# Optimization experiments

Measured on AMD Instinct MI355X. Metric: run time of the kernel, lower is better.

The kernel has to match this reference:

```python
import jax, jax.numpy as jnp
import numpy as np

N_NODES = 50000
NEG_SLOPE = 0.2

def _segment_softmax(e, seg, n):
    m = jax.ops.segment_max(e, seg, num_segments=n)
    ex = jnp.exp(e - m[seg])
    s = jax.ops.segment_sum(ex, seg, num_segments=n)
    return ex / s[seg]

def _gatv2_layer(x, src, dst, n, Wl, bl, Wr, br, att):
    # GATv2 (heads=1): e_ij = att . leaky_relu(Wl x_j + Wr x_i); msg = alpha * Wl x_j
    xl = x @ Wl + bl            # [N, D] source transform
    xr = x @ Wr + br            # [N, D] target transform
    h = jax.nn.leaky_relu(xl[src] + xr[dst], NEG_SLOPE)  # [E, D]
    e = h @ att                 # [E]
    alpha = _segment_softmax(e, dst, n)
    out = jax.ops.segment_sum(alpha[:, None] * xl[src], dst, num_segments=n)
    return out

def setup_inputs() -> dict:
    key = jax.random.key(0)
    ks = jax.random.split(key, 16)
    N, E, Q, F, D, H = N_NODES, 800000, 200000, 128, 250, 256
    def glorot(k, shape):
        fan = shape[0] + shape[-1]
        return jax.random.uniform(k, shape, jnp.float32, -1.0, 1.0) * np.sqrt(6.0 / fan)
    return {
        "x": jax.random.normal(ks[0], (N, F), jnp.float32),
        "edge_index": jax.random.randint(ks[1], (2, E), 0, N, jnp.int32),
        "query": jax.random.randint(ks[2], (Q, 2), 0, N, jnp.int32),
        "W1l": glorot(ks[3], (F, D)), "b1l": jnp.zeros((D,), jnp.float32),
        "W1r": glorot(ks[4], (F, D)), "b1r": jnp.zeros((D,), jnp.float32),
        "att1": glorot(ks[5], (D,)),
        "W2l": glorot(ks[6], (D, D)), "b2l": jnp.zeros((D,), jnp.float32),
        "W2r": glorot(ks[7], (D, D)), "b2r": jnp.zeros((D,), jnp.float32),
        "att2": glorot(ks[8], (D,)),
        "Wm1": glorot(ks[9], (2 * D, H)), "bm1": jnp.zeros((H,), jnp.float32),
        "Wm2": glorot(ks[10], (H, 1)), "bm2": jnp.zeros((1,), jnp.float32),
    }

def reference(x, edge_index, query, W1l, b1l, W1r, b1r, att1,
              W2l, b2l, W2r, b2r, att2, Wm1, bm1, Wm2, bm2):
    n = x.shape[0]
    # add self loops (PyG default add_self_loops=True)
    loops = jnp.arange(n, dtype=edge_index.dtype)
    src = jnp.concatenate([edge_index[0], loops])
    dst = jnp.concatenate([edge_index[1], loops])
    h = _gatv2_layer(x, src, dst, n, W1l, b1l, W1r, b1r, att1)
    h = jax.nn.relu(h)
    emb = _gatv2_layer(h, src, dst, n, W2l, b2l, W2r, b2r, att2)
    # edge-prediction head: gather pair embeddings, concat, MLP
    pair = jnp.concatenate([emb[query[:, 0]], emb[query[:, 1]]], axis=1)  # [Q, 2D]
    out = jax.nn.relu(pair @ Wm1 + bm1)
    out = jax.nn.relu(out @ Wm2 + bm2)
    return out
```

## Files before the change

### kernel.cpp

```cpp
#include <hip/hip_runtime.h>
#include <hip/hip_fp16.h>
#include <math.h>
#include <stdint.h>

#define NN 50000
#define NE 800000
#define ET (NE + NN)
#define FIN 128
#define DD 250
#define HD 256
#define NQ 200000
#define NEG_SLOPE 0.2f

typedef unsigned short u16;
typedef __attribute__((ext_vector_type(4))) float f32x4;
typedef _Float16 h2v __attribute__((ext_vector_type(2)));
typedef _Float16 f16x8 __attribute__((ext_vector_type(8)));

union H2U { h2v h; unsigned int u; };

__device__ __forceinline__ u16 f2h(float v) {
    __half h = __float2half(v);
    return *reinterpret_cast<u16*>(&h);
}
__device__ __forceinline__ float4 ld4h(const u16* p) {
    uint2 r = *(const uint2*)p;
    __half2 a = *(__half2*)&r.x;
    __half2 b = *(__half2*)&r.y;
    float2 fa = __half22float2(a), fb = __half22float2(b);
    return make_float4(fa.x, fa.y, fb.x, fb.y);
}
__device__ __forceinline__ h2v hmax2v(h2v a, h2v b) {
    return __builtin_elementwise_max(a, b);
}


__global__ void count_kernel(const int* __restrict__ ei, int* __restrict__ cnt) {
    int k = blockIdx.x * 256 + threadIdx.x;
    if (k >= ET) return;
    int d = (k < NE) ? ei[NE + k] : (k - NE);
    atomicAdd(&cnt[d], 1);
}

__global__ __launch_bounds__(256) void scan1_kernel(
    int* __restrict__ cnt, int* __restrict__ rowptr, int* __restrict__ bsum)
{
    __shared__ int buf[256];
    int t = threadIdx.x;
    int i = blockIdx.x * 256 + t;
    int v = (i < NN) ? cnt[i] : 0;
    if (i < NN) cnt[i] = 0;
    buf[t] = v;
    __syncthreads();
#pragma unroll
    for (int off = 1; off < 256; off <<= 1) {
        int add = (t >= off) ? buf[t - off] : 0;
        __syncthreads();
        buf[t] += add;
        __syncthreads();
    }
    if (i < NN) rowptr[i] = buf[t] - v;
    if (t == 255) bsum[blockIdx.x] = buf[255];
}

__global__ __launch_bounds__(256) void scan2_kernel(
    int* __restrict__ bsum, int* __restrict__ rowptr, int nb)
{
    __shared__ int buf[256];
    int t = threadIdx.x;
    int v = (t < nb) ? bsum[t] : 0;
    buf[t] = v;
    __syncthreads();
#pragma unroll
    for (int off = 1; off < 256; off <<= 1) {
        int add = (t >= off) ? buf[t - off] : 0;
        __syncthreads();
        buf[t] += add;
        __syncthreads();
    }
    if (t < nb) bsum[t] = buf[t] - v;
    if (t == 255) rowptr[NN] = buf[255];
}

__global__ __launch_bounds__(256) void scan3_kernel(
    int* __restrict__ rowptr, const int* __restrict__ bsum)
{
    int i = blockIdx.x * 256 + threadIdx.x;
    if (i < NN) rowptr[i] += bsum[blockIdx.x];
}

__global__ void scatter_kernel(const int* __restrict__ ei,
                               const int* __restrict__ rowptr,
                               int* __restrict__ fill,
                               int* __restrict__ ssrc) {
    int k = blockIdx.x * 256 + threadIdx.x;
    if (k >= ET) return;
    int s, d;
    if (k < NE) { s = ei[k]; d = ei[NE + k]; }
    else        { s = k - NE; d = k - NE; }
    int pos = rowptr[d] + atomicAdd(&fill[d], 1);
    ssrc[pos] = s << 9;
}


#define CONVX_BLOCKS 3125

__global__ __launch_bounds__(256) void conv_all(
    const float* __restrict__ x, int* __restrict__ fill,
    u16* __restrict__ Asp,
    const float* __restrict__ W1l, const float* __restrict__ W1r,
    const float* __restrict__ W2l, const float* __restrict__ W2r,
    const float* __restrict__ Wm1,
    u16* __restrict__ W1lT, u16* __restrict__ W1rT,
    u16* __restrict__ W2lT, u16* __restrict__ W2rT,
    u16* __restrict__ WmtT, u16* __restrict__ WmbT)
{
    if (blockIdx.x < CONVX_BLOCKS) {
        int tid = blockIdx.x * 256 + threadIdx.x;
        if (tid < NN) fill[tid] = 0;
        size_t idx = (size_t)tid * 8;
        if (idx >= (size_t)NN * FIN) return;
        float4 v0 = *(const float4*)(x + idx);
        float4 v1 = *(const float4*)(x + idx + 4);
        ushort4 o0, o1;
        o0.x = f2h(v0.x); o0.y = f2h(v0.y); o0.z = f2h(v0.z); o0.w = f2h(v0.w);
        o1.x = f2h(v1.x); o1.y = f2h(v1.y); o1.z = f2h(v1.z); o1.w = f2h(v1.w);
        *(ushort4*)(Asp + idx) = o0;
        *(ushort4*)(Asp + idx + 4) = o1;
        return;
    }
    int b = blockIdx.x - CONVX_BLOCKS;
    const float* W; int K, N, koff, kshift, b0; u16* ot;
    if (b < 128)       { W = W1l; K = FIN; N = DD; koff = 0;  kshift = 7; b0 = 0;    ot = W1lT; }
    else if (b < 256)  { W = W1r; K = FIN; N = DD; koff = 0;  kshift = 7; b0 = 128;  ot = W1rT; }
    else if (b < 512)  { W = W2l; K = DD;  N = DD; koff = 0;  kshift = 8; b0 = 256;  ot = W2lT; }
    else if (b < 768)  { W = W2r; K = DD;  N = DD; koff = 0;  kshift = 8; b0 = 512;  ot = W2rT; }
    else if (b < 1024) { W = Wm1; K = DD;  N = HD; koff = 0;  kshift = 8; b0 = 768;  ot = WmtT; }
    else               { W = Wm1; K = DD;  N = HD; koff = DD; kshift = 8; b0 = 1024; ot = WmbT; }
    int id = (b - b0) * 256 + threadIdx.x;
    int Kp = 1 << kshift;
    int n = id >> kshift, k = id & (Kp - 1);
    float v = (n < N && k < K) ? W[(size_t)(k + koff) * N + n] : 0.f;
    ot[id] = f2h(v);
}


#define AP 40

__global__ __launch_bounds__(256, 2) void gemm_pair(
    const u16* __restrict__ A, int Kp,
    const u16* __restrict__ B0, const u16* __restrict__ B1,
    const float* __restrict__ bias0, const float* __restrict__ bias1,
    void* __restrict__ C0v, void* __restrict__ C1v, int M, int N, int fmt)
{
    __shared__ u16 AS[128][AP], B0S[128][AP], B1S[128][AP];

    int row0 = blockIdx.x * 128;
    int col0 = blockIdx.y * 128;
    int t = threadIdx.x;
    int lane = t & 63, w = t >> 6;
    int wr = w >> 1, wc = w & 1;
    int quad = lane >> 4, rr = lane & 15;

    f32x4 acc0[4][4], acc1[4][4];
#pragma unroll
    for (int i = 0; i < 4; i++)
#pragma unroll
        for (int j = 0; j < 4; j++) {
            acc0[i][j] = (f32x4){0.f, 0.f, 0.f, 0.f};
            acc1[i][j] = (f32x4){0.f, 0.f, 0.f, 0.f};
        }

    int ar = t >> 1, akh = (t & 1) * 16;
    int gr = row0 + ar;
    int nB = col0 + ar;
    const u16* pA  = A  + (size_t)gr * Kp + akh;
    const u16* pB0 = B0 + (size_t)nB * Kp + akh;
    const u16* pB1 = B1 + (size_t)nB * Kp + akh;

    for (int k0 = 0; k0 < Kp; k0 += 32) {
        f16x8 a0{}, a1{};
        if (gr < M) {
            a0 = *(const f16x8*)(pA + k0);
            a1 = *(const f16x8*)(pA + k0 + 8);
        }
        *(f16x8*)&AS[ar][akh]      = a0;
        *(f16x8*)&AS[ar][akh + 8]  = a1;
        *(f16x8*)&B0S[ar][akh]     = *(const f16x8*)(pB0 + k0);
        *(f16x8*)&B0S[ar][akh + 8] = *(const f16x8*)(pB0 + k0 + 8);
        *(f16x8*)&B1S[ar][akh]     = *(const f16x8*)(pB1 + k0);
        *(f16x8*)&B1S[ar][akh + 8] = *(const f16x8*)(pB1 + k0 + 8);
        __syncthreads();

        f16x8 fA[4];
#pragma unroll
        for (int fi = 0; fi < 4; fi++) {
            int r = wr * 64 + fi * 16 + rr;
            fA[fi] = *(const f16x8*)&AS[r][quad * 8];
        }
#pragma unroll
        for (int fj = 0; fj < 4; fj++) {
            int c = wc * 64 + fj * 16 + rr;
            f16x8 b0 = *(const f16x8*)&B0S[c][quad * 8];
            f16x8 b1 = *(const f16x8*)&B1S[c][quad * 8];
#pragma unroll
            for (int fi = 0; fi < 4; fi++) {
                acc0[fi][fj] = __builtin_amdgcn_mfma_f32_16x16x32_f16(fA[fi], b0, acc0[fi][fj], 0, 0, 0);
                acc1[fi][fj] = __builtin_amdgcn_mfma_f32_16x16x32_f16(fA[fi], b1, acc1[fi][fj], 0, 0, 0);
            }
        }
        __syncthreads();
    }

#pragma unroll
    for (int fj = 0; fj < 4; fj++) {
        int gc = col0 + wc * 64 + fj * 16 + rr;
        if (gc >= N) continue;
        float bb0 = bias0 ? bias0[gc] : 0.f;
        float bb1 = bias1 ? bias1[gc] : 0.f;
#pragma unroll
        for (int fi = 0; fi < 4; fi++) {
#pragma unroll
            for (int r = 0; r < 4; r++) {
                int grr = row0 + wr * 64 + fi * 16 + quad * 4 + r;
                if (grr < M) {
                    float v0 = acc0[fi][fj][r] + bb0;
                    float v1 = acc1[fi][fj][r] + bb1;
                    if (fmt & 1) ((u16*)C0v)[(size_t)grr * 256 + gc] = f2h(v0);
                    else         ((float*)C0v)[(size_t)grr * N + gc] = v0;
                    if (fmt & 2) ((u16*)C1v)[(size_t)grr * 256 + gc] = f2h(v1);
                    else         ((float*)C1v)[(size_t)grr * N + gc] = v1;
                }
            }
        }
    }
}


__global__ __launch_bounds__(256) void fused_edge_kernel(
    const int* __restrict__ rowptr, const int* __restrict__ ssrc,
    const u16* __restrict__ xl16, const u16* __restrict__ xr16,
    const float* __restrict__ att,
    u16* __restrict__ Oh, int dorelu)
{
    int i = blockIdx.x * 4 + (threadIdx.x >> 6);
    if (i >= NN) return;
    int lane = threadIdx.x & 63;
    int beg = __builtin_amdgcn_readfirstlane(rowptr[i]);
    int end = __builtin_amdgcn_readfirstlane(rowptr[i + 1]);
    int d0 = lane * 4;
    int lb = d0 * 2;

    uint2 xrr = *(const uint2*)&xr16[(size_t)i * 256 + d0];
    h2v xr0h = *(h2v*)&xrr.x, xr1h = *(h2v*)&xrr.y;
    float atf[4] = {0.f, 0.f, 0.f, 0.f};
#pragma unroll
    for (int j = 0; j < 4; j++)
        if (d0 + j < DD) atf[j] = att[d0 + j];
    h2v at0h, at1h;
    at0h.x = (_Float16)atf[0]; at0h.y = (_Float16)atf[1];
    at1h.x = (_Float16)atf[2]; at1h.y = (_Float16)atf[3];
    const h2v c02 = {(_Float16)0.2f, (_Float16)0.2f};

    const char* xlb = (const char*)xl16;

    float m = -1e30f, ssum = 0.f;
    float4 acc = make_float4(0.f, 0.f, 0.f, 0.f);

    int p = beg;
    for (; p + 3 < end; p += 4) {
        int o0 = __builtin_amdgcn_readfirstlane(ssrc[p]);
        int o1 = __builtin_amdgcn_readfirstlane(ssrc[p + 1]);
        int o2 = __builtin_amdgcn_readfirstlane(ssrc[p + 2]);
        int o3 = __builtin_amdgcn_readfirstlane(ssrc[p + 3]);
        uint2 r0 = *(const uint2*)(xlb + o0 + lb);
        uint2 r1 = *(const uint2*)(xlb + o1 + lb);
        uint2 r2 = *(const uint2*)(xlb + o2 + lb);
        uint2 r3 = *(const uint2*)(xlb + o3 + lb);
        h2v x00 = *(h2v*)&r0.x, x01 = *(h2v*)&r0.y;
        h2v x10 = *(h2v*)&r1.x, x11 = *(h2v*)&r1.y;
        h2v x20 = *(h2v*)&r2.x, x21 = *(h2v*)&r2.y;
        h2v x30 = *(h2v*)&r3.x, x31 = *(h2v*)&r3.y;

        h2v s;
        float e0, e1, e2, e3;
        s = x00 + xr0h; s = hmax2v(s, s * c02);
        e0 = __builtin_amdgcn_fdot2(s, at0h, 0.f, false);
        s = x01 + xr1h; s = hmax2v(s, s * c02);
        e0 = __builtin_amdgcn_fdot2(s, at1h, e0, false);
        s = x10 + xr0h; s = hmax2v(s, s * c02);
        e1 = __builtin_amdgcn_fdot2(s, at0h, 0.f, false);
        s = x11 + xr1h; s = hmax2v(s, s * c02);
        e1 = __builtin_amdgcn_fdot2(s, at1h, e1, false);
        s = x20 + xr0h; s = hmax2v(s, s * c02);
        e2 = __builtin_amdgcn_fdot2(s, at0h, 0.f, false);
        s = x21 + xr1h; s = hmax2v(s, s * c02);
        e2 = __builtin_amdgcn_fdot2(s, at1h, e2, false);
        s = x30 + xr0h; s = hmax2v(s, s * c02);
        e3 = __builtin_amdgcn_fdot2(s, at0h, 0.f, false);
        s = x31 + xr1h; s = hmax2v(s, s * c02);
        e3 = __builtin_amdgcn_fdot2(s, at1h, e3, false);

        H2U u01, u23;
        u01.h.x = (_Float16)e0; u01.h.y = (_Float16)e1;
        u23.h.x = (_Float16)e2; u23.h.y = (_Float16)e3;
#pragma unroll
        for (int off = 1; off < 64; off <<= 1) {
            H2U t01, t23;
            t01.u = (unsigned int)__shfl_xor((int)u01.u, off, 64);
            t23.u = (unsigned int)__shfl_xor((int)u23.u, off, 64);
            u01.h = u01.h + t01.h;
            u23.h = u23.h + t23.h;
        }
        float es0 = (float)u01.h.x, es1 = (float)u01.h.y;
        float es2 = (float)u23.h.x, es3 = (float)u23.h.y;

        float nm = fmaxf(fmaxf(m, es0), fmaxf(fmaxf(es1, es2), es3));
        float sc = __expf(m - nm);
        float w0 = __expf(es0 - nm);
        float w1 = __expf(es1 - nm);
        float w2 = __expf(es2 - nm);
        float w3 = __expf(es3 - nm);
        float ax0 = fmaf(w1, (float)x10.x, w0 * (float)x00.x);
        float ax1 = fmaf(w3, (float)x30.x, w2 * (float)x20.x);
        float ay0 = fmaf(w1, (float)x10.y, w0 * (float)x00.y);
        float ay1 = fmaf(w3, (float)x30.y, w2 * (float)x20.y);
        float az0 = fmaf(w1, (float)x11.x, w0 * (float)x01.x);
        float az1 = fmaf(w3, (float)x31.x, w2 * (float)x21.x);
        float aw0 = fmaf(w1, (float)x11.y, w0 * (float)x01.y);
        float aw1 = fmaf(w3, (float)x31.y, w2 * (float)x21.y);
        acc.x = fmaf(acc.x, sc, ax0 + ax1);
        acc.y = fmaf(acc.y, sc, ay0 + ay1);
        acc.z = fmaf(acc.z, sc, az0 + az1);
        acc.w = fmaf(acc.w, sc, aw0 + aw1);
        ssum = fmaf(ssum, sc, (w0 + w1) + (w2 + w3));
        m = nm;
    }
    for (; p < end; p++) {
        int o = __builtin_amdgcn_readfirstlane(ssrc[p]);
        uint2 r = *(const uint2*)(xlb + o + lb);
        h2v x0 = *(h2v*)&r.x, x1 = *(h2v*)&r.y;
        h2v s;
        float e;
        s = x0 + xr0h; s = hmax2v(s, s * c02);
        e = __builtin_amdgcn_fdot2(s, at0h, 0.f, false);
        s = x1 + xr1h; s = hmax2v(s, s * c02);
        e = __builtin_amdgcn_fdot2(s, at1h, e, false);
#pragma unroll
        for (int off = 1; off < 64; off <<= 1)
            e += __shfl_xor(e, off, 64);
        float nm = fmaxf(m, e);
        float sc = __expf(m - nm);
        float w = __expf(e - nm);
        acc.x = fmaf(w, (float)x0.x, acc.x * sc);
        acc.y = fmaf(w, (float)x0.y, acc.y * sc);
        acc.z = fmaf(w, (float)x1.x, acc.z * sc);
        acc.w = fmaf(w, (float)x1.y, acc.w * sc);
        ssum = fmaf(ssum, sc, w);
        m = nm;
    }

    float inv = 1.f / ssum;
    acc.x *= inv; acc.y *= inv; acc.z *= inv; acc.w *= inv;
    if (dorelu) {
        acc.x = fmaxf(acc.x, 0.f); acc.y = fmaxf(acc.y, 0.f);
        acc.z = fmaxf(acc.z, 0.f); acc.w = fmaxf(acc.w, 0.f);
    }
    size_t base = (size_t)i * 256 + d0;
    ushort4 hv;
    hv.x = f2h(acc.x); hv.y = f2h(acc.y); hv.z = f2h(acc.z); hv.w = f2h(acc.w);
    *(ushort4*)&Oh[base] = hv;
}


__global__ __launch_bounds__(256) void query_kernel(
    const int* __restrict__ qry, const u16* __restrict__ Ptop,
    const u16* __restrict__ Pbot, const float* __restrict__ Wm2,
    const float* __restrict__ bm2, float* __restrict__ out)
{
    int q = (blockIdx.x * 4 + (threadIdx.x >> 6)) * 2;
    if (q >= NQ) return;
    int lane = threadIdx.x & 63;
    int a0 = __builtin_amdgcn_readfirstlane(qry[q * 2 + 0]);
    int b0 = __builtin_amdgcn_readfirstlane(qry[q * 2 + 1]);
    int a1 = __builtin_amdgcn_readfirstlane(qry[q * 2 + 2]);
    int b1 = __builtin_amdgcn_readfirstlane(qry[q * 2 + 3]);
    float4 w  = *(const float4*)&Wm2[lane * 4];
    float4 t0 = ld4h(&Ptop[(size_t)a0 * HD + lane * 4]);
    float4 v0 = ld4h(&Pbot[(size_t)b0 * HD + lane * 4]);
    float4 t1 = ld4h(&Ptop[(size_t)a1 * HD + lane * 4]);
    float4 v1 = ld4h(&Pbot[(size_t)b1 * HD + lane * 4]);
    float s0 = fmaxf(t0.x + v0.x, 0.f) * w.x + fmaxf(t0.y + v0.y, 0.f) * w.y
             + fmaxf(t0.z + v0.z, 0.f) * w.z + fmaxf(t0.w + v0.w, 0.f) * w.w;
    float s1 = fmaxf(t1.x + v1.x, 0.f) * w.x + fmaxf(t1.y + v1.y, 0.f) * w.y
             + fmaxf(t1.z + v1.z, 0.f) * w.z + fmaxf(t1.w + v1.w, 0.f) * w.w;
#pragma unroll
    for (int off = 32; off > 0; off >>= 1) {
        s0 += __shfl_down(s0, off, 64);
        s1 += __shfl_down(s1, off, 64);
    }
    if (lane == 0) {
        float bb = bm2[0];
        out[q] = fmaxf(s0 + bb, 0.f);
        if (q + 1 < NQ) out[q + 1] = fmaxf(s1 + bb, 0.f);
    }
}


extern "C" void kernel_launch(void* const* d_in, const int* in_sizes, int n_in,
                              void* d_out, int out_size, void* d_ws, size_t ws_size,
                              hipStream_t stream) {
    const float* x    = (const float*)d_in[0];
    const int*   ei   = (const int*)d_in[1];
    const int*   qry  = (const int*)d_in[2];
    const float* W1l  = (const float*)d_in[3];
    const float* b1l  = (const float*)d_in[4];
    const float* W1r  = (const float*)d_in[5];
    const float* b1r  = (const float*)d_in[6];
    const float* att1 = (const float*)d_in[7];
    const float* W2l  = (const float*)d_in[8];
    const float* b2l  = (const float*)d_in[9];
    const float* W2r  = (const float*)d_in[10];
    const float* b2r  = (const float*)d_in[11];
    const float* att2 = (const float*)d_in[12];
    const float* Wm1  = (const float*)d_in[13];
    const float* bm1  = (const float*)d_in[14];
    const float* Wm2  = (const float*)d_in[15];
    const float* bm2  = (const float*)d_in[16];
    float* out = (float*)d_out;

    u16* xl16    = (u16*)d_ws;
    u16* xr16    = xl16 + (size_t)NN * 256;
    int* rowptr  = (int*)(xr16 + (size_t)NN * 256);
    int* fill    = rowptr + NN + 1;
    int* ssrc    = fill + NN;
    int* bsum    = ssrc + ET;
    uintptr_t wp = (uintptr_t)(bsum + 256);
    wp = (wp + 63) & ~(uintptr_t)63;
    u16* W1lT = (u16*)wp;
    u16* W1rT = W1lT + 256 * 128;
    u16* W2lT = W1rT + 256 * 128;
    u16* W2rT = W2lT + 65536;
    u16* WmtT = W2rT + 65536;
    u16* WmbT = WmtT + 65536;
    u16* Asp  = WmbT + 65536;
    u16* Ptop16 = xl16;
    u16* Pbot16 = xr16;

    dim3 blk(256);
    int gET = (ET + 255) / 256;
    int gNode = (NN + 3) / 4;
    int nb = (NN + 255) / 256;
    dim3 gg((NN + 127) / 128, 2);

    conv_all<<<CONVX_BLOCKS + 1280, blk, 0, stream>>>(x, fill, Asp,
        W1l, W1r, W2l, W2r, Wm1,
        W1lT, W1rT, W2lT, W2rT, WmtT, WmbT);

    count_kernel<<<gET, blk, 0, stream>>>(ei, fill);
    scan1_kernel<<<nb, blk, 0, stream>>>(fill, rowptr, bsum);
    scan2_kernel<<<1, blk, 0, stream>>>(bsum, rowptr, nb);
    scan3_kernel<<<nb, blk, 0, stream>>>(rowptr, bsum);
    scatter_kernel<<<gET, blk, 0, stream>>>(ei, rowptr, fill, ssrc);

    gemm_pair<<<gg, blk, 0, stream>>>(Asp, 128, W1lT, W1rT,
                                      b1l, b1r, (void*)xl16, (void*)xr16, NN, DD, 3);
    fused_edge_kernel<<<gNode, blk, 0, stream>>>(rowptr, ssrc, xl16, xr16, att1, Asp, 1);

    gemm_pair<<<gg, blk, 0, stream>>>(Asp, 256, W2lT, W2rT,
                                      b2l, b2r, (void*)xl16, (void*)xr16, NN, DD, 3);
    fused_edge_kernel<<<gNode, blk, 0, stream>>>(rowptr, ssrc, xl16, xr16, att2, Asp, 0);

    gemm_pair<<<gg, blk, 0, stream>>>(Asp, 256, WmtT, WmbT,
                                      bm1, (const float*)nullptr, (void*)Ptop16, (void*)Pbot16, NN, HD, 3);

    query_kernel<<<(NQ / 2 + 3) / 4, blk, 0, stream>>>(qry, Ptop16, Pbot16, Wm2, bm2, out);
}
```

Before: 523.3 us.

## Software-pipeline edge gathers and use DPP wave reductions in aggregation

The per-node aggregation loop now prefetches the next group of four source rows and the following group's indices while computing the current group, so gather latency overlaps with the score and softmax math. The xor-shuffle butterfly reductions are replaced by DPP row shifts and row broadcasts followed by a readlane of lane 63, which avoids LDS-based shuffles. The query head uses the same DPP reduction. The 1-3 leftover edges are processed with their loads issued together. This raises register pressure and adds more complex control flow.

```diff
diff --git a/kernel.cpp b/kernel.cpp
--- a/kernel.cpp
+++ b/kernel.cpp
@@ -32,6 +32,34 @@
 }
 __device__ __forceinline__ h2v hmax2v(h2v a, h2v b) {
     return __builtin_elementwise_max(a, b);
+}
+
+
+#define DPPMOV(v, ctrl, rm) \
+    ((unsigned int)__builtin_amdgcn_update_dpp(0, (int)(v), (ctrl), (rm), 0xF, true))
+
+__device__ __forceinline__ unsigned int h2_wave_sum63(h2v x) {
+    H2U u, t; u.h = x;
+    t.u = DPPMOV(u.u, 0x111, 0xF); u.h = u.h + t.h;
+    t.u = DPPMOV(u.u, 0x112, 0xF); u.h = u.h + t.h;
+    t.u = DPPMOV(u.u, 0x114, 0xF); u.h = u.h + t.h;
+    t.u = DPPMOV(u.u, 0x118, 0xF); u.h = u.h + t.h;
+    t.u = DPPMOV(u.u, 0x142, 0xA); u.h = u.h + t.h;
+    t.u = DPPMOV(u.u, 0x143, 0xC); u.h = u.h + t.h;
+    return (unsigned int)__builtin_amdgcn_readlane((int)u.u, 63);
+}
+
+__device__ __forceinline__ float f32_wave_sum63(float x) {
+    union FU { float f; unsigned int u; } a, t, o;
+    a.f = x;
+    t.u = DPPMOV(a.u, 0x111, 0xF); a.f += t.f;
+    t.u = DPPMOV(a.u, 0x112, 0xF); a.f += t.f;
+    t.u = DPPMOV(a.u, 0x114, 0xF); a.f += t.f;
+    t.u = DPPMOV(a.u, 0x118, 0xF); a.f += t.f;
+    t.u = DPPMOV(a.u, 0x142, 0xA); a.f += t.f;
+    t.u = DPPMOV(a.u, 0x143, 0xC); a.f += t.f;
+    o.u = (unsigned int)__builtin_amdgcn_readlane((int)a.u, 63);
+    return o.f;
 }
 
 
@@ -267,88 +295,19 @@
     float m = -1e30f, ssum = 0.f;
     float4 acc = make_float4(0.f, 0.f, 0.f, 0.f);
 
-    int p = beg;
-    for (; p + 3 < end; p += 4) {
-        int o0 = __builtin_amdgcn_readfirstlane(ssrc[p]);
-        int o1 = __builtin_amdgcn_readfirstlane(ssrc[p + 1]);
-        int o2 = __builtin_amdgcn_readfirstlane(ssrc[p + 2]);
-        int o3 = __builtin_amdgcn_readfirstlane(ssrc[p + 3]);
-        uint2 r0 = *(const uint2*)(xlb + o0 + lb);
-        uint2 r1 = *(const uint2*)(xlb + o1 + lb);
-        uint2 r2 = *(const uint2*)(xlb + o2 + lb);
-        uint2 r3 = *(const uint2*)(xlb + o3 + lb);
-        h2v x00 = *(h2v*)&r0.x, x01 = *(h2v*)&r0.y;
-        h2v x10 = *(h2v*)&r1.x, x11 = *(h2v*)&r1.y;
-        h2v x20 = *(h2v*)&r2.x, x21 = *(h2v*)&r2.y;
-        h2v x30 = *(h2v*)&r3.x, x31 = *(h2v*)&r3.y;
-
-        h2v s;
-        float e0, e1, e2, e3;
-        s = x00 + xr0h; s = hmax2v(s, s * c02);
-        e0 = __builtin_amdgcn_fdot2(s, at0h, 0.f, false);
-        s = x01 + xr1h; s = hmax2v(s, s * c02);
-        e0 = __builtin_amdgcn_fdot2(s, at1h, e0, false);
-        s = x10 + xr0h; s = hmax2v(s, s * c02);
-        e1 = __builtin_amdgcn_fdot2(s, at0h, 0.f, false);
-        s = x11 + xr1h; s = hmax2v(s, s * c02);
-        e1 = __builtin_amdgcn_fdot2(s, at1h, e1, false);
-        s = x20 + xr0h; s = hmax2v(s, s * c02);
-        e2 = __builtin_amdgcn_fdot2(s, at0h, 0.f, false);
-        s = x21 + xr1h; s = hmax2v(s, s * c02);
-        e2 = __builtin_amdgcn_fdot2(s, at1h, e2, false);
-        s = x30 + xr0h; s = hmax2v(s, s * c02);
-        e3 = __builtin_amdgcn_fdot2(s, at0h, 0.f, false);
-        s = x31 + xr1h; s = hmax2v(s, s * c02);
-        e3 = __builtin_amdgcn_fdot2(s, at1h, e3, false);
-
-        H2U u01, u23;
-        u01.h.x = (_Float16)e0; u01.h.y = (_Float16)e1;
-        u23.h.x = (_Float16)e2; u23.h.y = (_Float16)e3;
-#pragma unroll
-        for (int off = 1; off < 64; off <<= 1) {
-            H2U t01, t23;
-            t01.u = (unsigned int)__shfl_xor((int)u01.u, off, 64);
-            t23.u = (unsigned int)__shfl_xor((int)u23.u, off, 64);
-            u01.h = u01.h + t01.h;
-            u23.h = u23.h + t23.h;
-        }
-        float es0 = (float)u01.h.x, es1 = (float)u01.h.y;
-        float es2 = (float)u23.h.x, es3 = (float)u23.h.y;
-
-        float nm = fmaxf(fmaxf(m, es0), fmaxf(fmaxf(es1, es2), es3));
-        float sc = __expf(m - nm);
-        float w0 = __expf(es0 - nm);
-        float w1 = __expf(es1 - nm);
-        float w2 = __expf(es2 - nm);
-        float w3 = __expf(es3 - nm);
-        float ax0 = fmaf(w1, (float)x10.x, w0 * (float)x00.x);
-        float ax1 = fmaf(w3, (float)x30.x, w2 * (float)x20.x);
-        float ay0 = fmaf(w1, (float)x10.y, w0 * (float)x00.y);
-        float ay1 = fmaf(w3, (float)x30.y, w2 * (float)x20.y);
-        float az0 = fmaf(w1, (float)x11.x, w0 * (float)x01.x);
-        float az1 = fmaf(w3, (float)x31.x, w2 * (float)x21.x);
-        float aw0 = fmaf(w1, (float)x11.y, w0 * (float)x01.y);
-        float aw1 = fmaf(w3, (float)x31.y, w2 * (float)x21.y);
-        acc.x = fmaf(acc.x, sc, ax0 + ax1);
-        acc.y = fmaf(acc.y, sc, ay0 + ay1);
-        acc.z = fmaf(acc.z, sc, az0 + az1);
-        acc.w = fmaf(acc.w, sc, aw0 + aw1);
-        ssum = fmaf(ssum, sc, (w0 + w1) + (w2 + w3));
-        m = nm;
-    }
-    for (; p < end; p++) {
-        int o = __builtin_amdgcn_readfirstlane(ssrc[p]);
-        uint2 r = *(const uint2*)(xlb + o + lb);
-        h2v x0 = *(h2v*)&r.x, x1 = *(h2v*)&r.y;
-        h2v s;
-        float e;
-        s = x0 + xr0h; s = hmax2v(s, s * c02);
-        e = __builtin_amdgcn_fdot2(s, at0h, 0.f, false);
+    auto ldrow = [&](int o) -> uint2 {
+        return *(const uint2*)(xlb + o + lb);
+    };
+    auto edge_score = [&](uint2 g) -> float {
+        h2v x0 = *(h2v*)&g.x, x1 = *(h2v*)&g.y;
+        h2v s = x0 + xr0h; s = hmax2v(s, s * c02);
+        float e = __builtin_amdgcn_fdot2(s, at0h, 0.f, false);
         s = x1 + xr1h; s = hmax2v(s, s * c02);
-        e = __builtin_amdgcn_fdot2(s, at1h, e, false);
-#pragma unroll
-        for (int off = 1; off < 64; off <<= 1)
-            e += __shfl_xor(e, off, 64);
+        return __builtin_amdgcn_fdot2(s, at1h, e, false);
+    };
+    auto single_update = [&](uint2 g) {
+        float e = f32_wave_sum63(edge_score(g));
+        h2v x0 = *(h2v*)&g.x, x1 = *(h2v*)&g.y;
         float nm = fmaxf(m, e);
         float sc = __expf(m - nm);
         float w = __expf(e - nm);
@@ -358,6 +317,111 @@
         acc.w = fmaf(w, (float)x1.y, acc.w * sc);
         ssum = fmaf(ssum, sc, w);
         m = nm;
+    };
+
+    int p = beg;
+    if (p + 3 < end) {
+        int o0 = __builtin_amdgcn_readfirstlane(ssrc[p]);
+        int o1 = __builtin_amdgcn_readfirstlane(ssrc[p + 1]);
+        int o2 = __builtin_amdgcn_readfirstlane(ssrc[p + 2]);
+        int o3 = __builtin_amdgcn_readfirstlane(ssrc[p + 3]);
+        uint2 c0 = ldrow(o0), c1 = ldrow(o1), c2 = ldrow(o2), c3 = ldrow(o3);
+        bool hn = (p + 7 < end);
+        int no0 = 0, no1 = 0, no2 = 0, no3 = 0;
+        if (hn) {
+            no0 = __builtin_amdgcn_readfirstlane(ssrc[p + 4]);
+            no1 = __builtin_amdgcn_readfirstlane(ssrc[p + 5]);
+            no2 = __builtin_amdgcn_readfirstlane(ssrc[p + 6]);
+            no3 = __builtin_amdgcn_readfirstlane(ssrc[p + 7]);
+        }
+        for (;;) {
+            uint2 n0, n1, n2, n3;
+            if (hn) {
+                n0 = ldrow(no0); n1 = ldrow(no1); n2 = ldrow(no2); n3 = ldrow(no3);
+            }
+            bool hnn = (p + 11 < end);
+            int nn0 = 0, nn1 = 0, nn2 = 0, nn3 = 0;
+            if (hnn) {
+                nn0 = __builtin_amdgcn_readfirstlane(ssrc[p + 8]);
+                nn1 = __builtin_amdgcn_readfirstlane(ssrc[p + 9]);
+                nn2 = __builtin_amdgcn_readfirstlane(ssrc[p + 10]);
+                nn3 = __builtin_amdgcn_readfirstlane(ssrc[p + 11]);
+            }
+
+            h2v x00 = *(h2v*)&c0.x, x01 = *(h2v*)&c0.y;
+            h2v x10 = *(h2v*)&c1.x, x11 = *(h2v*)&c1.y;
+            h2v x20 = *(h2v*)&c2.x, x21 = *(h2v*)&c2.y;
+            h2v x30 = *(h2v*)&c3.x, x31 = *(h2v*)&c3.y;
+
+            h2v s;
+            float e0, e1, e2, e3;
+            s = x00 + xr0h; s = hmax2v(s, s * c02);
+            e0 = __builtin_amdgcn_fdot2(s, at0h, 0.f, false);
+            s = x01 + xr1h; s = hmax2v(s, s * c02);
+            e0 = __builtin_amdgcn_fdot2(s, at1h, e0, false);
+            s = x10 + xr0h; s = hmax2v(s, s * c02);
+            e1 = __builtin_amdgcn_fdot2(s, at0h, 0.f, false);
+            s = x11 + xr1h; s = hmax2v(s, s * c02);
+            e1 = __builtin_amdgcn_fdot2(s, at1h, e1, false);
+            s = x20 + xr0h; s = hmax2v(s, s * c02);
+            e2 = __builtin_amdgcn_fdot2(s, at0h, 0.f, false);
+            s = x21 + xr1h; s = hmax2v(s, s * c02);
+            e2 = __builtin_amdgcn_fdot2(s, at1h, e2, false);
+            s = x30 + xr0h; s = hmax2v(s, s * c02);
+            e3 = __builtin_amdgcn_fdot2(s, at0h, 0.f, false);
+            s = x31 + xr1h; s = hmax2v(s, s * c02);
+            e3 = __builtin_amdgcn_fdot2(s, at1h, e3, false);
+
+            H2U u01, u23, r01, r23;
+            u01.h.x = (_Float16)e0; u01.h.y = (_Float16)e1;
+            u23.h.x = (_Float16)e2; u23.h.y = (_Float16)e3;
+            r01.u = h2_wave_sum63(u01.h);
+            r23.u = h2_wave_sum63(u23.h);
+            float es0 = (float)r01.h.x, es1 = (float)r01.h.y;
+            float es2 = (float)r23.h.x, es3 = (float)r23.h.y;
+
+            float nm = fmaxf(fmaxf(m, es0), fmaxf(fmaxf(es1, es2), es3));
+            float sc = __expf(m - nm);
+            float w0 = __expf(es0 - nm);
+            float w1 = __expf(es1 - nm);
+            float w2 = __expf(es2 - nm);
+            float w3 = __expf(es3 - nm);
+            float ax0 = fmaf(w1, (float)x10.x, w0 * (float)x00.x);
+            float ax1 = fmaf(w3, (float)x30.x, w2 * (float)x20.x);
+            float ay0 = fmaf(w1, (float)x10.y, w0 * (float)x00.y);
+            float ay1 = fmaf(w3, (float)x30.y, w2 * (float)x20.y);
+            float az0 = fmaf(w1, (float)x11.x, w0 * (float)x01.x);
+            float az1 = fmaf(w3, (float)x31.x, w2 * (float)x21.x);
+            float aw0 = fmaf(w1, (float)x11.y, w0 * (float)x01.y);
+            float aw1 = fmaf(w3, (float)x31.y, w2 * (float)x21.y);
+            acc.x = fmaf(acc.x, sc, ax0 + ax1);
+            acc.y = fmaf(acc.y, sc, ay0 + ay1);
+            acc.z = fmaf(acc.z, sc, az0 + az1);
+            acc.w = fmaf(acc.w, sc, aw0 + aw1);
+            ssum = fmaf(ssum, sc, (w0 + w1) + (w2 + w3));
+            m = nm;
+
+            p += 4;
+            if (!hn) break;
+            c0 = n0; c1 = n1; c2 = n2; c3 = n3;
+            no0 = nn0; no1 = nn1; no2 = nn2; no3 = nn3;
+            hn = hnn;
+        }
+    }
+
+    int rem = end - p;
+    if (rem > 0) {
+        int o0 = __builtin_amdgcn_readfirstlane(ssrc[p]);
+        int o1 = 0, o2 = 0;
+        if (rem > 1) o1 = __builtin_amdgcn_readfirstlane(ssrc[p + 1]);
+        if (rem > 2) o2 = __builtin_amdgcn_readfirstlane(ssrc[p + 2]);
+        uint2 g0 = ldrow(o0);
+        uint2 g1, g2;
+        if (rem > 1) g1 = ldrow(o1);
+        if (rem > 2) g2 = ldrow(o2);
+        single_update(g0);
+        if (rem > 1) single_update(g1);
+        if (rem > 2) single_update(g2);
     }
 
     float inv = 1.f / ssum;
@@ -394,11 +458,8 @@
              + fmaxf(t0.z + v0.z, 0.f) * w.z + fmaxf(t0.w + v0.w, 0.f) * w.w;
     float s1 = fmaxf(t1.x + v1.x, 0.f) * w.x + fmaxf(t1.y + v1.y, 0.f) * w.y
              + fmaxf(t1.z + v1.z, 0.f) * w.z + fmaxf(t1.w + v1.w, 0.f) * w.w;
-#pragma unroll
-    for (int off = 32; off > 0; off >>= 1) {
-        s0 += __shfl_down(s0, off, 64);
-        s1 += __shfl_down(s1, off, 64);
-    }
+    s0 = f32_wave_sum63(s0);
+    s1 = f32_wave_sum63(s1);
     if (lane == 0) {
         float bb = bm2[0];
         out[q] = fmaxf(s0 + bb, 0.f);
```

Measured after the change: 522.0 us. No clear change (-0.2%).
